# Kernel tuning notes

Measured on AMD Instinct MI355X. Metric: run time of the kernel, lower is better.

The kernel has to match this reference:

```python
import jax, jax.numpy as jnp
import numpy as np

L, H, D, DH, N, B, V, PAD = 6, 8, 512, 64, 300, 64, 32000, 0
DFF = 4 * D

def _layernorm(x, g, b):
    m = x.mean(-1, keepdims=True)
    v = ((x - m) ** 2).mean(-1, keepdims=True)
    return (x - m) * jax.lax.rsqrt(v + 1e-5) * g + b

def setup_inputs() -> dict:
    key = jax.random.key(0)
    ks = jax.random.split(key, 8)
    emb = jax.random.normal(ks[0], (V, D), dtype=jnp.float32) * 0.02
    emb = emb.at[PAD].set(0.0)  # padding_idx row is zero
    pos = jax.random.normal(ks[1], (N, D), dtype=jnp.float32) * 0.02
    Wk = jax.random.normal(ks[2], (L, H, D, DH), dtype=jnp.float32) * 0.02  # shared K=Q=V proj (module bug: uses self.key for all three)
    Wo = jax.random.normal(ks[3], (L, D, D), dtype=jnp.float32) * 0.02
    W1 = jax.random.normal(ks[4], (L, D, DFF), dtype=jnp.float32) * 0.02
    b1 = jnp.zeros((L, DFF), dtype=jnp.float32)
    W2 = jax.random.normal(ks[5], (L, DFF, D), dtype=jnp.float32) * 0.02
    b2 = jnp.zeros((L, D), dtype=jnp.float32)
    gamma = jnp.ones((L, D), dtype=jnp.float32)   # ONE LayerNorm per block, shared for both norms
    beta = jnp.zeros((L, D), dtype=jnp.float32)
    tokens = jax.random.randint(ks[6], (B, N), 0, V)
    return dict(tokens=tokens, emb=emb, pos=pos, Wk=Wk, Wo=Wo, W1=W1, b1=b1, W2=W2, b2=b2, gamma=gamma, beta=beta)

def reference(tokens, emb, pos, Wk, Wo, W1, b1, W2, b2, gamma, beta):
    x = emb[tokens] + pos[: tokens.shape[1]]  # [B,N,D]
    scale = 1.0 / jnp.sqrt(jnp.asarray(D, x.dtype))  # divides by sqrt(512), NOT sqrt(head_dim)
    for l in range(L):
        k = jnp.einsum('bnd,hde->bhne', x, Wk[l])          # Q=K=V  [B,H,N,DH]
        s = jnp.einsum('bhne,bhme->bhnm', k, k) * scale    # [B,H,N,N]
        a = jax.nn.softmax(s, axis=-1)
        o = jnp.einsum('bhnm,bhme->bhne', a, k)            # [B,H,N,DH]
        o = o.transpose(0, 2, 1, 3).reshape(x.shape[0], x.shape[1], D)
        z = _layernorm(o @ Wo[l] + x, gamma[l], beta[l])
        h = jax.nn.relu(z @ W1[l] + b1[l]) @ W2[l] + b2[l]
        x = _layernorm(h + z, gamma[l], beta[l])
    return x
```

## Files before the change

### kernel.cpp

```cpp
#include <hip/hip_runtime.h>

#define L_LAYERS 6
#define HEADS    8
#define DMODEL   512
#define DHEAD    64
#define SEQ      300
#define BATCH    64
#define DFFN     2048
#define BN_ROWS  (BATCH*SEQ)
#define NPAD     320

typedef __bf16 bf16_t;
typedef bf16_t bf16x8 __attribute__((ext_vector_type(8)));
typedef bf16_t bf16x4 __attribute__((ext_vector_type(4)));
typedef float  f32x4  __attribute__((ext_vector_type(4)));

#define GLOAD16(gp, lp) __builtin_amdgcn_global_load_lds( \
    (__attribute__((address_space(1))) void*)(gp),        \
    (__attribute__((address_space(3))) void*)(lp), 16, 0, 0)

__global__ __launch_bounds__(256) void transpose_w8(const float* __restrict__ w,
                                                    bf16_t* __restrict__ o,
                                                    int K, int Nc)
{
    int idx = blockIdx.x * 256 + threadIdx.x;
    int n   = idx % Nc;
    int r   = idx / Nc;
    int k8  = (r % (K / 8)) * 8;
    int l   = r / (K / 8);
    const float* wp = w + (size_t)l * K * Nc + (size_t)k8 * Nc + n;
    bf16x8 t;
#pragma unroll
    for (int j = 0; j < 8; ++j) t[j] = (bf16_t)wp[(size_t)j * Nc];
    *(bf16x8*)(o + (size_t)l * K * Nc + (size_t)n * K + k8) = t;
}

__global__ __launch_bounds__(256) void transpose_wk8(const float* __restrict__ wk,
                                                     bf16_t* __restrict__ o)
{
    int idx = blockIdx.x * 256 + threadIdx.x;
    int e  = idx % DHEAD;
    int r  = idx / DHEAD;
    int d8 = (r % (DMODEL / 8)) * 8;
    r      = r / (DMODEL / 8);
    int h  = r % HEADS;
    int l  = r / HEADS;
    const float* wp = wk + (((size_t)(l * HEADS + h) * DMODEL + d8) * DHEAD + e);
    bf16x8 t;
#pragma unroll
    for (int j = 0; j < 8; ++j) t[j] = (bf16_t)wp[(size_t)j * DHEAD];
    *(bf16x8*)(o + (size_t)l * DMODEL * DMODEL + (size_t)(h * DHEAD + e) * DMODEL + d8) = t;
}

__global__ __launch_bounds__(128) void embed_k(const int* __restrict__ tok,
                                               const float* __restrict__ emb,
                                               const float* __restrict__ pos,
                                               bf16_t* __restrict__ xb)
{
    int row = blockIdx.x;
    int n   = row % SEQ;
    int tkn = tok[row];
    int c   = threadIdx.x * 4;
    float4 e = *(const float4*)(emb + (size_t)tkn * DMODEL + c);
    float4 p = *(const float4*)(pos + (size_t)n * DMODEL + c);
    bf16x4 o;
    o[0] = (bf16_t)(e.x + p.x); o[1] = (bf16_t)(e.y + p.y);
    o[2] = (bf16_t)(e.z + p.z); o[3] = (bf16_t)(e.w + p.w);
    *(bf16x4*)(xb + (size_t)row * DMODEL + c) = o;
}

template <int EPI, typename OUT_T>
__global__ __launch_bounds__(256) void gemm_bt(const bf16_t* __restrict__ A,
                                               const bf16_t* __restrict__ BT,
                                               OUT_T* __restrict__ C,
                                               const float* __restrict__ bias,
                                               const bf16_t* __restrict__ resid,
                                               int M, int K, int Nc, int tiles_n)
{
    __shared__ bf16_t As[128 * 64];
    __shared__ bf16_t Bs[128 * 64];
    const int t    = threadIdx.x;
    const int tm   = blockIdx.x / tiles_n;
    const int tn   = blockIdx.x % tiles_n;
    const int lane = t & 63, wid = t >> 6;
    const int wr   = wid >> 1, wc = wid & 1;
    const int fr   = lane & 15, fq = lane >> 4;

    const f32x4 FZ = {0.f, 0.f, 0.f, 0.f};
    f32x4 acc[4][4];
#pragma unroll
    for (int m = 0; m < 4; ++m)
#pragma unroll
        for (int n = 0; n < 4; ++n) acc[m][n] = FZ;

    const bf16_t* Ab = A  + (size_t)tm * 128 * K;
    const bf16_t* Bb = BT + (size_t)tn * 128 * K;

    for (int k0 = 0; k0 < K; k0 += 64) {
#pragma unroll
        for (int i = 0; i < 4; ++i) {
            int idx8 = (i * 256 + t) * 8;
            int row  = idx8 >> 6;
            int colg = (idx8 & 63) ^ ((row & 7) << 3);
            GLOAD16(Ab + (size_t)row * K + k0 + colg, As + idx8);
            GLOAD16(Bb + (size_t)row * K + k0 + colg, Bs + idx8);
        }
        __syncthreads();
#pragma unroll
        for (int kk = 0; kk < 2; ++kk) {
            bf16x8 af[4], bfr[4];
#pragma unroll
            for (int m = 0; m < 4; ++m) {
                int row = wr * 64 + m * 16 + fr;
                af[m] = *(const bf16x8*)(As + row * 64 + ((kk * 32 + fq * 8) ^ ((row & 7) << 3)));
            }
#pragma unroll
            for (int n = 0; n < 4; ++n) {
                int row = wc * 64 + n * 16 + fr;
                bfr[n] = *(const bf16x8*)(Bs + row * 64 + ((kk * 32 + fq * 8) ^ ((row & 7) << 3)));
            }
#pragma unroll
            for (int m = 0; m < 4; ++m)
#pragma unroll
                for (int n = 0; n < 4; ++n)
                    acc[m][n] = __builtin_amdgcn_mfma_f32_16x16x32_bf16(af[m], bfr[n], acc[m][n], 0, 0, 0);
        }
        __syncthreads();
    }

#pragma unroll
    for (int m = 0; m < 4; ++m) {
#pragma unroll
        for (int n = 0; n < 4; ++n) {
            int colg = tn * 128 + wc * 64 + n * 16 + fr;
            float bv = (EPI == 2 || EPI == 3) ? bias[colg] : 0.f;
#pragma unroll
            for (int r = 0; r < 4; ++r) {
                int rowg = tm * 128 + wr * 64 + m * 16 + fq * 4 + r;
                float v = acc[m][n][r] + bv;
                if (EPI == 2) v = fmaxf(v, 0.f);
                if (EPI == 1 || EPI == 3) v += (float)resid[(size_t)rowg * Nc + colg];
                C[(size_t)rowg * Nc + colg] = (OUT_T)v;
            }
        }
    }
}

__global__ __launch_bounds__(256) void attn_k(const bf16_t* __restrict__ kin,
                                              bf16_t* __restrict__ out)
{
    __shared__ bf16_t Kl[NPAD * 64];
    __shared__ bf16_t KT[64 * NPAD];
    __shared__ bf16_t Pl[4 * 16 * NPAD];

    const int bh = blockIdx.x;
    const int b  = bh >> 3, h = bh & 7;
    const bf16_t* kbase = kin + (size_t)b * SEQ * DMODEL + h * DHEAD;
    const int t  = threadIdx.x;
    const int rr = t >> 3;
    const int cg = (t & 7) * 8;

    for (int pass = 0; pass < NPAD / 32; ++pass) {
        int row = pass * 32 + rr;
        bf16x8 v;
        if (row < SEQ) v = *(const bf16x8*)(kbase + (size_t)row * DMODEL + cg);
        else {
#pragma unroll
            for (int j = 0; j < 8; ++j) v[j] = (bf16_t)0.f;
        }
        *(bf16x8*)(Kl + row * 64 + (cg ^ ((row & 7) << 3))) = v;
#pragma unroll
        for (int j = 0; j < 8; ++j) {
            int col = cg + j;
            KT[col * NPAD + (row ^ ((col & 7) << 3))] = v[j];
        }
    }
    __syncthreads();

    const int lane = t & 63, w = t >> 6;
    const int fr = lane & 15, fq = lane >> 4;
    const float scale = 0.044194173824159216f;
    const f32x4 FZ = {0.f, 0.f, 0.f, 0.f};

    for (int i = 0; i < 5; ++i) {
        int qt = w * 5 + i;
        f32x4 s[20];
#pragma unroll
        for (int ct = 0; ct < 20; ++ct) s[ct] = FZ;
#pragma unroll
        for (int kk = 0; kk < 2; ++kk) {
            int qrow = qt * 16 + fr;
            bf16x8 aq = *(const bf16x8*)(Kl + qrow * 64 + ((kk * 32 + fq * 8) ^ ((qrow & 7) << 3)));
#pragma unroll
            for (int ct = 0; ct < 20; ++ct) {
                int krow = ct * 16 + fr;
                bf16x8 bk = *(const bf16x8*)(Kl + krow * 64 + ((kk * 32 + fq * 8) ^ ((krow & 7) << 3)));
                s[ct] = __builtin_amdgcn_mfma_f32_16x16x32_bf16(aq, bk, s[ct], 0, 0, 0);
            }
        }
#pragma unroll
        for (int r = 0; r < 4; ++r) {
            float mx = -1e30f;
#pragma unroll
            for (int ct = 0; ct < 20; ++ct) {
                float v = s[ct][r] * scale;
                if (ct * 16 + fr < SEQ) mx = fmaxf(mx, v);
            }
            mx = fmaxf(mx, __shfl_xor(mx, 1));
            mx = fmaxf(mx, __shfl_xor(mx, 2));
            mx = fmaxf(mx, __shfl_xor(mx, 4));
            mx = fmaxf(mx, __shfl_xor(mx, 8));
            float p[20];
            float sm = 0.f;
#pragma unroll
            for (int ct = 0; ct < 20; ++ct) {
                float v = (ct * 16 + fr < SEQ) ? __expf(s[ct][r] * scale - mx) : 0.f;
                p[ct] = v; sm += v;
            }
            sm += __shfl_xor(sm, 1); sm += __shfl_xor(sm, 2);
            sm += __shfl_xor(sm, 4); sm += __shfl_xor(sm, 8);
            float rinv = 1.f / sm;
            int pr = fq * 4 + r;
#pragma unroll
            for (int ct = 0; ct < 20; ++ct) {
                int col = ct * 16 + fr;
                Pl[(w * 16 + pr) * NPAD + (col ^ ((pr & 7) << 3))] = (bf16_t)(p[ct] * rinv);
            }
        }
#pragma unroll
        for (int n = 0; n < 4; ++n) {
            f32x4 oacc = FZ;
#pragma unroll
            for (int kk = 0; kk < 10; ++kk) {
                bf16x8 ap = *(const bf16x8*)(Pl + (w * 16 + fr) * NPAD + ((kk * 32 + fq * 8) ^ ((fr & 7) << 3)));
                int dr = n * 16 + fr;
                bf16x8 bv = *(const bf16x8*)(KT + dr * NPAD + ((kk * 32 + fq * 8) ^ ((dr & 7) << 3)));
                oacc = __builtin_amdgcn_mfma_f32_16x16x32_bf16(ap, bv, oacc, 0, 0, 0);
            }
#pragma unroll
            for (int r = 0; r < 4; ++r) {
                int qrow = qt * 16 + fq * 4 + r;
                if (qrow < SEQ)
                    out[(size_t)(b * SEQ + qrow) * DMODEL + h * DHEAD + n * 16 + fr] = (bf16_t)oacc[r];
            }
        }
    }
}

template <bool FINAL>
__global__ __launch_bounds__(256) void ln_k(const float* __restrict__ in,
                                            const float* __restrict__ gam,
                                            const float* __restrict__ bet,
                                            bf16_t* __restrict__ outb,
                                            float* __restrict__ outf)
{
    int row  = blockIdx.x * 4 + (threadIdx.x >> 6);
    int lane = threadIdx.x & 63;
    const float* x = in + (size_t)row * DMODEL + lane * 8;
    float4 v0 = *(const float4*)x;
    float4 v1 = *(const float4*)(x + 4);
    float s  = v0.x + v0.y + v0.z + v0.w + v1.x + v1.y + v1.z + v1.w;
    float s2 = v0.x * v0.x + v0.y * v0.y + v0.z * v0.z + v0.w * v0.w
             + v1.x * v1.x + v1.y * v1.y + v1.z * v1.z + v1.w * v1.w;
#pragma unroll
    for (int m = 1; m < 64; m <<= 1) { s += __shfl_xor(s, m); s2 += __shfl_xor(s2, m); }
    float mean = s * (1.f / DMODEL);
    float rstd = rsqrtf(s2 * (1.f / DMODEL) - mean * mean + 1e-5f);
    float4 g0 = *(const float4*)(gam + lane * 8), g1 = *(const float4*)(gam + lane * 8 + 4);
    float4 b0 = *(const float4*)(bet + lane * 8), b1 = *(const float4*)(bet + lane * 8 + 4);
    float y[8];
    y[0] = (v0.x - mean) * rstd * g0.x + b0.x;
    y[1] = (v0.y - mean) * rstd * g0.y + b0.y;
    y[2] = (v0.z - mean) * rstd * g0.z + b0.z;
    y[3] = (v0.w - mean) * rstd * g0.w + b0.w;
    y[4] = (v1.x - mean) * rstd * g1.x + b1.x;
    y[5] = (v1.y - mean) * rstd * g1.y + b1.y;
    y[6] = (v1.z - mean) * rstd * g1.z + b1.z;
    y[7] = (v1.w - mean) * rstd * g1.w + b1.w;
    bf16x8 ob;
#pragma unroll
    for (int j = 0; j < 8; ++j) ob[j] = (bf16_t)y[j];
    *(bf16x8*)(outb + (size_t)row * DMODEL + lane * 8) = ob;
    if (FINAL) {
        float4 o0 = {y[0], y[1], y[2], y[3]};
        float4 o1 = {y[4], y[5], y[6], y[7]};
        *(float4*)(outf + (size_t)row * DMODEL + lane * 8)     = o0;
        *(float4*)(outf + (size_t)row * DMODEL + lane * 8 + 4) = o1;
    }
}

extern "C" void kernel_launch(void* const* d_in, const int* in_sizes, int n_in,
                              void* d_out, int out_size, void* d_ws, size_t ws_size,
                              hipStream_t stream)
{
    const int*   tok = (const int*)d_in[0];
    const float* emb = (const float*)d_in[1];
    const float* pos = (const float*)d_in[2];
    const float* Wk  = (const float*)d_in[3];
    const float* Wo  = (const float*)d_in[4];
    const float* W1  = (const float*)d_in[5];
    const float* b1  = (const float*)d_in[6];
    const float* W2  = (const float*)d_in[7];
    const float* b2  = (const float*)d_in[8];
    const float* gam = (const float*)d_in[9];
    const float* bet = (const float*)d_in[10];
    float* outp = (float*)d_out;

    char* ws = (char*)d_ws;
    size_t off = 0;
    auto alloc = [&](size_t bytes) {
        off = (off + 255) & ~(size_t)255;
        void* p = ws + off;
        off += bytes;
        return p;
    };
    bf16_t* WKT  = (bf16_t*)alloc((size_t)L_LAYERS * DMODEL * DMODEL * 2);
    bf16_t* WOT  = (bf16_t*)alloc((size_t)L_LAYERS * DMODEL * DMODEL * 2);
    bf16_t* W1T  = (bf16_t*)alloc((size_t)L_LAYERS * DMODEL * DFFN * 2);
    bf16_t* W2T  = (bf16_t*)alloc((size_t)L_LAYERS * DMODEL * DFFN * 2);
    bf16_t* buf0 = (bf16_t*)alloc((size_t)BN_ROWS * DMODEL * 2);
    bf16_t* buf1 = (bf16_t*)alloc((size_t)BN_ROWS * DMODEL * 2);
    bf16_t* kb   = (bf16_t*)alloc((size_t)BN_ROWS * DMODEL * 2);
    bf16_t* ob   = (bf16_t*)alloc((size_t)BN_ROWS * DMODEL * 2);
    bf16_t* h1b  = (bf16_t*)alloc((size_t)BN_ROWS * DFFN * 2);
    float*  tf   = (float*)alloc((size_t)BN_ROWS * DMODEL * 4);

    transpose_wk8<<<768, 256, 0, stream>>>(Wk, WKT);
    transpose_w8<<<768, 256, 0, stream>>>(Wo, WOT, DMODEL, DMODEL);
    transpose_w8<<<3072, 256, 0, stream>>>(W1, W1T, DMODEL, DFFN);
    transpose_w8<<<3072, 256, 0, stream>>>(W2, W2T, DFFN, DMODEL);

    embed_k<<<BN_ROWS, 128, 0, stream>>>(tok, emb, pos, buf0);

    for (int l = 0; l < L_LAYERS; ++l) {
        gemm_bt<0, bf16_t><<<150 * 4, 256, 0, stream>>>(
            buf0, WKT + (size_t)l * DMODEL * DMODEL, kb, nullptr, nullptr,
            BN_ROWS, DMODEL, DMODEL, 4);
        attn_k<<<BATCH * HEADS, 256, 0, stream>>>(kb, ob);
        gemm_bt<1, float><<<150 * 4, 256, 0, stream>>>(
            ob, WOT + (size_t)l * DMODEL * DMODEL, tf, nullptr, buf0,
            BN_ROWS, DMODEL, DMODEL, 4);
        ln_k<false><<<BN_ROWS / 4, 256, 0, stream>>>(
            tf, gam + l * DMODEL, bet + l * DMODEL, buf1, nullptr);
        gemm_bt<2, bf16_t><<<150 * 16, 256, 0, stream>>>(
            buf1, W1T + (size_t)l * DMODEL * DFFN, h1b, b1 + l * DFFN, nullptr,
            BN_ROWS, DMODEL, DFFN, 16);
        gemm_bt<3, float><<<150 * 4, 256, 0, stream>>>(
            h1b, W2T + (size_t)l * DMODEL * DFFN, tf, b2 + l * DMODEL, buf1,
            BN_ROWS, DFFN, DMODEL, 4);
        if (l < L_LAYERS - 1)
            ln_k<false><<<BN_ROWS / 4, 256, 0, stream>>>(
                tf, gam + l * DMODEL, bet + l * DMODEL, buf0, nullptr);
        else
            ln_k<true><<<BN_ROWS / 4, 256, 0, stream>>>(
                tf, gam + l * DMODEL, bet + l * DMODEL, buf0, outp);
    }
}
```

Measured before the change: 1.786 ms.

## Replace GEMM with 256x256-tile double-buffered pipelined kernel and XCD-aware tile mapping

Replaces the 128x128 single-buffered GEMM with a 512-thread, 256x256-tile kernel that double-buffers A and B in LDS. Loads for the next K-tile are issued in phases interleaved with MFMA work, using explicit vmcnt waits, barriers and setprio. It also remaps block IDs so contiguous tiles land on the same XCD, and uses larger tiles to raise per-block data reuse. The cost is 128KB of LDS per block and fewer blocks: grids drop to 150 or 600 on a 256-CU part, which risks under-filling the GPU on the narrow GEMMs.

```diff
diff --git a/kernel.cpp b/kernel.cpp
--- a/kernel.cpp
+++ b/kernel.cpp
@@ -18,6 +18,10 @@
 #define GLOAD16(gp, lp) __builtin_amdgcn_global_load_lds( \
     (__attribute__((address_space(1))) void*)(gp),        \
     (__attribute__((address_space(3))) void*)(lp), 16, 0, 0)
+
+#define MEMBAR() asm volatile("" ::: "memory")
+#define PHASE_BAR() do { MEMBAR(); __builtin_amdgcn_s_barrier(); MEMBAR(); } while (0)
+#define VMCNT4() asm volatile("s_waitcnt vmcnt(4)" ::: "memory")
 
 __global__ __launch_bounds__(256) void transpose_w8(const float* __restrict__ w,
                                                     bf16_t* __restrict__ o,
@@ -70,77 +74,111 @@
 }
 
 template <int EPI, typename OUT_T>
-__global__ __launch_bounds__(256) void gemm_bt(const bf16_t* __restrict__ A,
-                                               const bf16_t* __restrict__ BT,
-                                               OUT_T* __restrict__ C,
-                                               const float* __restrict__ bias,
-                                               const bf16_t* __restrict__ resid,
-                                               int M, int K, int Nc, int tiles_n)
-{
-    __shared__ bf16_t As[128 * 64];
-    __shared__ bf16_t Bs[128 * 64];
-    const int t    = threadIdx.x;
-    const int tm   = blockIdx.x / tiles_n;
-    const int tn   = blockIdx.x % tiles_n;
+__global__ __launch_bounds__(512, 2) void gemm256(const bf16_t* __restrict__ A,
+                                                  const bf16_t* __restrict__ BT,
+                                                  OUT_T* __restrict__ C,
+                                                  const float* __restrict__ bias,
+                                                  const bf16_t* __restrict__ resid,
+                                                  int K, int Nc, int tiles_n)
+{
+    __shared__ bf16_t smem[65536];
+    bf16_t* As  = smem;
+    bf16_t* Bsm = smem + 32768;
+
+    const int t = threadIdx.x;
+    const int nwg = gridDim.x;
+    const int q = nwg >> 3, r = nwg & 7;
+    const int xc = blockIdx.x & 7, sq = blockIdx.x >> 3;
+    const int lt = (xc < r ? xc * (q + 1) : r * (q + 1) + (xc - r) * q) + sq;
+    const int tm = lt / tiles_n, tn = lt % tiles_n;
+
+    const bf16_t* Ab = A  + (size_t)tm * 256 * K;
+    const bf16_t* Bb = BT + (size_t)tn * 256 * K;
     const int lane = t & 63, wid = t >> 6;
-    const int wr   = wid >> 1, wc = wid & 1;
-    const int fr   = lane & 15, fq = lane >> 4;
+    const int wr = wid >> 2, wc = wid & 3;
+    const int fr = lane & 15, fq = lane >> 4;
+    const int NT = K >> 6;
+
+    auto stage_a = [&](int dbuf, int half, int kt) {
+#pragma unroll
+        for (int j = 0; j < 2; ++j) {
+            int idx8 = (j * 512 + t) * 8;
+            int rl   = idx8 >> 6;
+            int cg   = (idx8 & 63) ^ ((rl & 7) << 3);
+            GLOAD16(Ab + (size_t)(half * 128 + rl) * K + kt * 64 + cg,
+                    As + dbuf * 16384 + half * 8192 + idx8);
+        }
+    };
+    auto stage_b = [&](int dbuf, int nq, int kt) {
+#pragma unroll
+        for (int j = 0; j < 2; ++j) {
+            int idx8 = (j * 512 + t) * 8;
+            int rl   = idx8 >> 6;
+            int cg   = (idx8 & 63) ^ ((rl & 7) << 3);
+            int grow = (rl >> 5) * 64 + nq * 32 + (rl & 31);
+            GLOAD16(Bb + (size_t)grow * K + kt * 64 + cg,
+                    Bsm + dbuf * 16384 + nq * 8192 + idx8);
+        }
+    };
 
     const f32x4 FZ = {0.f, 0.f, 0.f, 0.f};
-    f32x4 acc[4][4];
-#pragma unroll
-    for (int m = 0; m < 4; ++m)
+    f32x4 acc[8][4];
+#pragma unroll
+    for (int m = 0; m < 8; ++m)
 #pragma unroll
         for (int n = 0; n < 4; ++n) acc[m][n] = FZ;
 
-    const bf16_t* Ab = A  + (size_t)tm * 128 * K;
-    const bf16_t* Bb = BT + (size_t)tn * 128 * K;
-
-    for (int k0 = 0; k0 < K; k0 += 64) {
-#pragma unroll
-        for (int i = 0; i < 4; ++i) {
-            int idx8 = (i * 256 + t) * 8;
-            int row  = idx8 >> 6;
-            int colg = (idx8 & 63) ^ ((row & 7) << 3);
-            GLOAD16(Ab + (size_t)row * K + k0 + colg, As + idx8);
-            GLOAD16(Bb + (size_t)row * K + k0 + colg, Bs + idx8);
-        }
-        __syncthreads();
-#pragma unroll
-        for (int kk = 0; kk < 2; ++kk) {
-            bf16x8 af[4], bfr[4];
-#pragma unroll
-            for (int m = 0; m < 4; ++m) {
-                int row = wr * 64 + m * 16 + fr;
-                af[m] = *(const bf16x8*)(As + row * 64 + ((kk * 32 + fq * 8) ^ ((row & 7) << 3)));
-            }
-#pragma unroll
-            for (int n = 0; n < 4; ++n) {
-                int row = wc * 64 + n * 16 + fr;
-                bfr[n] = *(const bf16x8*)(Bs + row * 64 + ((kk * 32 + fq * 8) ^ ((row & 7) << 3)));
-            }
-#pragma unroll
-            for (int m = 0; m < 4; ++m)
-#pragma unroll
-                for (int n = 0; n < 4; ++n)
-                    acc[m][n] = __builtin_amdgcn_mfma_f32_16x16x32_bf16(af[m], bfr[n], acc[m][n], 0, 0, 0);
-        }
-        __syncthreads();
-    }
-
-#pragma unroll
-    for (int m = 0; m < 4; ++m) {
+    stage_a(0, 0, 0); stage_a(0, 1, 0);
+    stage_b(0, 0, 0); stage_b(0, 1, 0);
+    stage_b(1, 0, 1);
+    VMCNT4();
+    PHASE_BAR();
+
+    for (int tt = 0; tt < NT; ++tt) {
+        const int buf = tt & 1, nbuf = buf ^ 1;
+        const bf16_t* Ap = As + buf * 16384 + (wr * 128 + fr) * 64;
+#pragma unroll
+        for (int ph = 0; ph < 4; ++ph) {
+            const int nq = ph >> 1, kk = ph & 1;
+            const int ca = (kk * 32 + fq * 8) ^ ((fr & 7) << 3);
+            bf16x8 af[8];
+#pragma unroll
+            for (int m = 0; m < 8; ++m)
+                af[m] = *(const bf16x8*)(Ap + m * 1024 + ca);
+            const bf16_t* Bp = Bsm + buf * 16384 + nq * 8192 + (wc * 32 + fr) * 64;
+            bf16x8 b0 = *(const bf16x8*)(Bp + ca);
+            bf16x8 b1 = *(const bf16x8*)(Bp + 1024 + ca);
+
+            if (ph == 0) { if (tt + 1 < NT) stage_a(nbuf, 0, tt + 1); }
+            if (ph == 1) { if (tt + 1 < NT) stage_a(nbuf, 1, tt + 1); VMCNT4(); }
+            if (ph == 2) { if (tt + 2 < NT) stage_b(buf, 0, tt + 2); }
+            if (ph == 3) { if (tt + 1 < NT) stage_b(nbuf, 1, tt + 1); VMCNT4(); }
+
+            PHASE_BAR();
+            __builtin_amdgcn_s_setprio(1);
+#pragma unroll
+            for (int m = 0; m < 8; ++m) {
+                acc[m][nq * 2]     = __builtin_amdgcn_mfma_f32_16x16x32_bf16(af[m], b0, acc[m][nq * 2], 0, 0, 0);
+                acc[m][nq * 2 + 1] = __builtin_amdgcn_mfma_f32_16x16x32_bf16(af[m], b1, acc[m][nq * 2 + 1], 0, 0, 0);
+            }
+            __builtin_amdgcn_s_setprio(0);
+            PHASE_BAR();
+        }
+    }
+
+#pragma unroll
+    for (int m = 0; m < 8; ++m) {
+        const int rowg = tm * 256 + wr * 128 + m * 16 + fq * 4;
 #pragma unroll
         for (int n = 0; n < 4; ++n) {
-            int colg = tn * 128 + wc * 64 + n * 16 + fr;
+            const int colg = tn * 256 + wc * 64 + n * 16 + fr;
             float bv = (EPI == 2 || EPI == 3) ? bias[colg] : 0.f;
 #pragma unroll
-            for (int r = 0; r < 4; ++r) {
-                int rowg = tm * 128 + wr * 64 + m * 16 + fq * 4 + r;
-                float v = acc[m][n][r] + bv;
+            for (int rr = 0; rr < 4; ++rr) {
+                float v = acc[m][n][rr] + bv;
                 if (EPI == 2) v = fmaxf(v, 0.f);
-                if (EPI == 1 || EPI == 3) v += (float)resid[(size_t)rowg * Nc + colg];
-                C[(size_t)rowg * Nc + colg] = (OUT_T)v;
+                if (EPI == 1 || EPI == 3) v += (float)resid[(size_t)(rowg + rr) * Nc + colg];
+                C[(size_t)(rowg + rr) * Nc + colg] = (OUT_T)v;
             }
         }
     }
@@ -333,21 +371,21 @@
     embed_k<<<BN_ROWS, 128, 0, stream>>>(tok, emb, pos, buf0);
 
     for (int l = 0; l < L_LAYERS; ++l) {
-        gemm_bt<0, bf16_t><<<150 * 4, 256, 0, stream>>>(
+        gemm256<0, bf16_t><<<75 * 2, 512, 0, stream>>>(
             buf0, WKT + (size_t)l * DMODEL * DMODEL, kb, nullptr, nullptr,
-            BN_ROWS, DMODEL, DMODEL, 4);
+            DMODEL, DMODEL, 2);
         attn_k<<<BATCH * HEADS, 256, 0, stream>>>(kb, ob);
-        gemm_bt<1, float><<<150 * 4, 256, 0, stream>>>(
+        gemm256<1, float><<<75 * 2, 512, 0, stream>>>(
             ob, WOT + (size_t)l * DMODEL * DMODEL, tf, nullptr, buf0,
-            BN_ROWS, DMODEL, DMODEL, 4);
+            DMODEL, DMODEL, 2);
         ln_k<false><<<BN_ROWS / 4, 256, 0, stream>>>(
             tf, gam + l * DMODEL, bet + l * DMODEL, buf1, nullptr);
-        gemm_bt<2, bf16_t><<<150 * 16, 256, 0, stream>>>(
+        gemm256<2, bf16_t><<<75 * 8, 512, 0, stream>>>(
             buf1, W1T + (size_t)l * DMODEL * DFFN, h1b, b1 + l * DFFN, nullptr,
-            BN_ROWS, DMODEL, DFFN, 16);
-        gemm_bt<3, float><<<150 * 4, 256, 0, stream>>>(
+            DMODEL, DFFN, 8);
+        gemm256<3, float><<<75 * 2, 512, 0, stream>>>(
             h1b, W2T + (size_t)l * DMODEL * DFFN, tf, b2 + l * DMODEL, buf1,
-            BN_ROWS, DFFN, DMODEL, 4);
+            DFFN, DMODEL, 2);
         if (l < L_LAYERS - 1)
             ln_k<false><<<BN_ROWS / 4, 256, 0, stream>>>(
                 tf, gam + l * DMODEL, bet + l * DMODEL, buf0, nullptr);
```

New measurement: 1.692 ms. 1.06x faster.

## Double-buffer GEMM LDS loads, remap tiles across XCDs, store pre-LN sums as bf16

Applied to the files above, without the earlier changes.

The GEMM now double-buffers its LDS tiles, so the next K-slice's global-to-LDS loads are issued while the current slice's MFMAs run, and one barrier per iteration replaces two. It also raises MFMA wave priority, sets two blocks per SM through launch bounds, and remaps block IDs so contiguous tiles land on the same XCD for L2 reuse. Separately, the residual-add output feeding LayerNorm is stored as bf16 instead of fp32, which halves that intermediate traffic. That adds extra rounding before the normalization.

```diff
diff --git a/kernel.cpp b/kernel.cpp
--- a/kernel.cpp
+++ b/kernel.cpp
@@ -18,6 +18,10 @@
 #define GLOAD16(gp, lp) __builtin_amdgcn_global_load_lds( \
     (__attribute__((address_space(1))) void*)(gp),        \
     (__attribute__((address_space(3))) void*)(lp), 16, 0, 0)
+
+#define MEMBAR() asm volatile("" ::: "memory")
+#define PHASE_BAR() do { MEMBAR(); __builtin_amdgcn_s_barrier(); MEMBAR(); } while (0)
+#define VMCNT0() asm volatile("s_waitcnt vmcnt(0)" ::: "memory")
 
 __global__ __launch_bounds__(256) void transpose_w8(const float* __restrict__ w,
                                                     bf16_t* __restrict__ o,
@@ -70,21 +74,40 @@
 }
 
 template <int EPI, typename OUT_T>
-__global__ __launch_bounds__(256) void gemm_bt(const bf16_t* __restrict__ A,
-                                               const bf16_t* __restrict__ BT,
-                                               OUT_T* __restrict__ C,
-                                               const float* __restrict__ bias,
-                                               const bf16_t* __restrict__ resid,
-                                               int M, int K, int Nc, int tiles_n)
-{
-    __shared__ bf16_t As[128 * 64];
-    __shared__ bf16_t Bs[128 * 64];
-    const int t    = threadIdx.x;
-    const int tm   = blockIdx.x / tiles_n;
-    const int tn   = blockIdx.x % tiles_n;
+__global__ __launch_bounds__(256, 2) void gemm128(const bf16_t* __restrict__ A,
+                                                  const bf16_t* __restrict__ BT,
+                                                  OUT_T* __restrict__ C,
+                                                  const float* __restrict__ bias,
+                                                  const bf16_t* __restrict__ resid,
+                                                  int K, int Nc, int tiles_n)
+{
+    __shared__ bf16_t smem[32768];
+    bf16_t* As = smem;
+    bf16_t* Bs = smem + 16384;
+
+    const int t = threadIdx.x;
+    const int nwg = gridDim.x;
+    const int q = nwg >> 3, r = nwg & 7;
+    const int xc = blockIdx.x & 7, sq = blockIdx.x >> 3;
+    const int lt = (xc < r ? xc * (q + 1) : r * (q + 1) + (xc - r) * q) + sq;
+    const int tm = lt / tiles_n, tn = lt % tiles_n;
+
+    const bf16_t* Ab = A  + (size_t)tm * 128 * K;
+    const bf16_t* Bb = BT + (size_t)tn * 128 * K;
     const int lane = t & 63, wid = t >> 6;
-    const int wr   = wid >> 1, wc = wid & 1;
-    const int fr   = lane & 15, fq = lane >> 4;
+    const int wr = wid >> 1, wc = wid & 1;
+    const int fr = lane & 15, fq = lane >> 4;
+    const int NT = K >> 6;
+
+    auto stage = [&](bf16_t* dst, const bf16_t* src, int kt) {
+#pragma unroll
+        for (int j = 0; j < 4; ++j) {
+            int idx8 = (j * 256 + t) * 8;
+            int rl   = idx8 >> 6;
+            int cg   = (idx8 & 63) ^ ((rl & 7) << 3);
+            GLOAD16(src + (size_t)rl * K + kt * 64 + cg, dst + idx8);
+        }
+    };
 
     const f32x4 FZ = {0.f, 0.f, 0.f, 0.f};
     f32x4 acc[4][4];
@@ -93,39 +116,40 @@
 #pragma unroll
         for (int n = 0; n < 4; ++n) acc[m][n] = FZ;
 
-    const bf16_t* Ab = A  + (size_t)tm * 128 * K;
-    const bf16_t* Bb = BT + (size_t)tn * 128 * K;
-
-    for (int k0 = 0; k0 < K; k0 += 64) {
-#pragma unroll
-        for (int i = 0; i < 4; ++i) {
-            int idx8 = (i * 256 + t) * 8;
-            int row  = idx8 >> 6;
-            int colg = (idx8 & 63) ^ ((row & 7) << 3);
-            GLOAD16(Ab + (size_t)row * K + k0 + colg, As + idx8);
-            GLOAD16(Bb + (size_t)row * K + k0 + colg, Bs + idx8);
-        }
-        __syncthreads();
-#pragma unroll
-        for (int kk = 0; kk < 2; ++kk) {
-            bf16x8 af[4], bfr[4];
-#pragma unroll
-            for (int m = 0; m < 4; ++m) {
-                int row = wr * 64 + m * 16 + fr;
-                af[m] = *(const bf16x8*)(As + row * 64 + ((kk * 32 + fq * 8) ^ ((row & 7) << 3)));
-            }
-#pragma unroll
-            for (int n = 0; n < 4; ++n) {
-                int row = wc * 64 + n * 16 + fr;
-                bfr[n] = *(const bf16x8*)(Bs + row * 64 + ((kk * 32 + fq * 8) ^ ((row & 7) << 3)));
-            }
-#pragma unroll
-            for (int m = 0; m < 4; ++m)
-#pragma unroll
-                for (int n = 0; n < 4; ++n)
-                    acc[m][n] = __builtin_amdgcn_mfma_f32_16x16x32_bf16(af[m], bfr[n], acc[m][n], 0, 0, 0);
-        }
-        __syncthreads();
+    stage(As, Ab, 0); stage(Bs, Bb, 0);
+    VMCNT0(); PHASE_BAR();
+
+    for (int tt = 0; tt < NT; ++tt) {
+        const int buf = tt & 1, nbuf = buf ^ 1;
+        const bf16_t* Ap = As + buf * 8192 + (wr * 64 + fr) * 64;
+        const bf16_t* Bp = Bs + buf * 8192 + (wc * 64 + fr) * 64;
+        const int ca0 = (fq * 8) ^ ((fr & 7) << 3);
+        const int ca1 = ca0 ^ 32;
+        bf16x8 af[4], bfr[4];
+#pragma unroll
+        for (int m = 0; m < 4; ++m) af[m] = *(const bf16x8*)(Ap + m * 1024 + ca0);
+#pragma unroll
+        for (int n = 0; n < 4; ++n) bfr[n] = *(const bf16x8*)(Bp + n * 1024 + ca0);
+        if (tt + 1 < NT) { stage(As + nbuf * 8192, Ab, tt + 1); stage(Bs + nbuf * 8192, Bb, tt + 1); }
+        __builtin_amdgcn_s_setprio(1);
+#pragma unroll
+        for (int m = 0; m < 4; ++m)
+#pragma unroll
+            for (int n = 0; n < 4; ++n)
+                acc[m][n] = __builtin_amdgcn_mfma_f32_16x16x32_bf16(af[m], bfr[n], acc[m][n], 0, 0, 0);
+        __builtin_amdgcn_s_setprio(0);
+#pragma unroll
+        for (int m = 0; m < 4; ++m) af[m] = *(const bf16x8*)(Ap + m * 1024 + ca1);
+#pragma unroll
+        for (int n = 0; n < 4; ++n) bfr[n] = *(const bf16x8*)(Bp + n * 1024 + ca1);
+        __builtin_amdgcn_s_setprio(1);
+#pragma unroll
+        for (int m = 0; m < 4; ++m)
+#pragma unroll
+            for (int n = 0; n < 4; ++n)
+                acc[m][n] = __builtin_amdgcn_mfma_f32_16x16x32_bf16(af[m], bfr[n], acc[m][n], 0, 0, 0);
+        __builtin_amdgcn_s_setprio(0);
+        VMCNT0(); PHASE_BAR();
     }
 
 #pragma unroll
@@ -135,9 +159,9 @@
             int colg = tn * 128 + wc * 64 + n * 16 + fr;
             float bv = (EPI == 2 || EPI == 3) ? bias[colg] : 0.f;
 #pragma unroll
-            for (int r = 0; r < 4; ++r) {
-                int rowg = tm * 128 + wr * 64 + m * 16 + fq * 4 + r;
-                float v = acc[m][n][r] + bv;
+            for (int rr2 = 0; rr2 < 4; ++rr2) {
+                int rowg = tm * 128 + wr * 64 + m * 16 + fq * 4 + rr2;
+                float v = acc[m][n][rr2] + bv;
                 if (EPI == 2) v = fmaxf(v, 0.f);
                 if (EPI == 1 || EPI == 3) v += (float)resid[(size_t)rowg * Nc + colg];
                 C[(size_t)rowg * Nc + colg] = (OUT_T)v;
@@ -248,7 +272,7 @@
 }
 
 template <bool FINAL>
-__global__ __launch_bounds__(256) void ln_k(const float* __restrict__ in,
+__global__ __launch_bounds__(256) void ln_k(const bf16_t* __restrict__ in,
                                             const float* __restrict__ gam,
                                             const float* __restrict__ bet,
                                             bf16_t* __restrict__ outb,
@@ -256,34 +280,36 @@
 {
     int row  = blockIdx.x * 4 + (threadIdx.x >> 6);
     int lane = threadIdx.x & 63;
-    const float* x = in + (size_t)row * DMODEL + lane * 8;
-    float4 v0 = *(const float4*)x;
-    float4 v1 = *(const float4*)(x + 4);
-    float s  = v0.x + v0.y + v0.z + v0.w + v1.x + v1.y + v1.z + v1.w;
-    float s2 = v0.x * v0.x + v0.y * v0.y + v0.z * v0.z + v0.w * v0.w
-             + v1.x * v1.x + v1.y * v1.y + v1.z * v1.z + v1.w * v1.w;
+    bf16x8 v = *(const bf16x8*)(in + (size_t)row * DMODEL + lane * 8);
+    float y[8];
+    float s = 0.f, s2 = 0.f;
+#pragma unroll
+    for (int j = 0; j < 8; ++j) {
+        float f = (float)v[j];
+        y[j] = f; s += f; s2 += f * f;
+    }
 #pragma unroll
     for (int m = 1; m < 64; m <<= 1) { s += __shfl_xor(s, m); s2 += __shfl_xor(s2, m); }
     float mean = s * (1.f / DMODEL);
     float rstd = rsqrtf(s2 * (1.f / DMODEL) - mean * mean + 1e-5f);
     float4 g0 = *(const float4*)(gam + lane * 8), g1 = *(const float4*)(gam + lane * 8 + 4);
     float4 b0 = *(const float4*)(bet + lane * 8), b1 = *(const float4*)(bet + lane * 8 + 4);
-    float y[8];
-    y[0] = (v0.x - mean) * rstd * g0.x + b0.x;
-    y[1] = (v0.y - mean) * rstd * g0.y + b0.y;
-    y[2] = (v0.z - mean) * rstd * g0.z + b0.z;
-    y[3] = (v0.w - mean) * rstd * g0.w + b0.w;
-    y[4] = (v1.x - mean) * rstd * g1.x + b1.x;
-    y[5] = (v1.y - mean) * rstd * g1.y + b1.y;
-    y[6] = (v1.z - mean) * rstd * g1.z + b1.z;
-    y[7] = (v1.w - mean) * rstd * g1.w + b1.w;
+    float z[8];
+    z[0] = (y[0] - mean) * rstd * g0.x + b0.x;
+    z[1] = (y[1] - mean) * rstd * g0.y + b0.y;
+    z[2] = (y[2] - mean) * rstd * g0.z + b0.z;
+    z[3] = (y[3] - mean) * rstd * g0.w + b0.w;
+    z[4] = (y[4] - mean) * rstd * g1.x + b1.x;
+    z[5] = (y[5] - mean) * rstd * g1.y + b1.y;
+    z[6] = (y[6] - mean) * rstd * g1.z + b1.z;
+    z[7] = (y[7] - mean) * rstd * g1.w + b1.w;
     bf16x8 ob;
 #pragma unroll
-    for (int j = 0; j < 8; ++j) ob[j] = (bf16_t)y[j];
+    for (int j = 0; j < 8; ++j) ob[j] = (bf16_t)z[j];
     *(bf16x8*)(outb + (size_t)row * DMODEL + lane * 8) = ob;
     if (FINAL) {
-        float4 o0 = {y[0], y[1], y[2], y[3]};
-        float4 o1 = {y[4], y[5], y[6], y[7]};
+        float4 o0 = {z[0], z[1], z[2], z[3]};
+        float4 o1 = {z[4], z[5], z[6], z[7]};
         *(float4*)(outf + (size_t)row * DMODEL + lane * 8)     = o0;
         *(float4*)(outf + (size_t)row * DMODEL + lane * 8 + 4) = o1;
     }
@@ -323,7 +349,7 @@
     bf16_t* kb   = (bf16_t*)alloc((size_t)BN_ROWS * DMODEL * 2);
     bf16_t* ob   = (bf16_t*)alloc((size_t)BN_ROWS * DMODEL * 2);
     bf16_t* h1b  = (bf16_t*)alloc((size_t)BN_ROWS * DFFN * 2);
-    float*  tf   = (float*)alloc((size_t)BN_ROWS * DMODEL * 4);
+    bf16_t* tfb  = (bf16_t*)alloc((size_t)BN_ROWS * DMODEL * 2);
 
     transpose_wk8<<<768, 256, 0, stream>>>(Wk, WKT);
     transpose_w8<<<768, 256, 0, stream>>>(Wo, WOT, DMODEL, DMODEL);
@@ -333,26 +359,26 @@
     embed_k<<<BN_ROWS, 128, 0, stream>>>(tok, emb, pos, buf0);
 
     for (int l = 0; l < L_LAYERS; ++l) {
-        gemm_bt<0, bf16_t><<<150 * 4, 256, 0, stream>>>(
+        gemm128<0, bf16_t><<<600, 256, 0, stream>>>(
             buf0, WKT + (size_t)l * DMODEL * DMODEL, kb, nullptr, nullptr,
-            BN_ROWS, DMODEL, DMODEL, 4);
+            DMODEL, DMODEL, 4);
         attn_k<<<BATCH * HEADS, 256, 0, stream>>>(kb, ob);
-        gemm_bt<1, float><<<150 * 4, 256, 0, stream>>>(
-            ob, WOT + (size_t)l * DMODEL * DMODEL, tf, nullptr, buf0,
-            BN_ROWS, DMODEL, DMODEL, 4);
+        gemm128<1, bf16_t><<<600, 256, 0, stream>>>(
+            ob, WOT + (size_t)l * DMODEL * DMODEL, tfb, nullptr, buf0,
+            DMODEL, DMODEL, 4);
         ln_k<false><<<BN_ROWS / 4, 256, 0, stream>>>(
-            tf, gam + l * DMODEL, bet + l * DMODEL, buf1, nullptr);
-        gemm_bt<2, bf16_t><<<150 * 16, 256, 0, stream>>>(
+            tfb, gam + l * DMODEL, bet + l * DMODEL, buf1, nullptr);
+        gemm128<2, bf16_t><<<2400, 256, 0, stream>>>(
             buf1, W1T + (size_t)l * DMODEL * DFFN, h1b, b1 + l * DFFN, nullptr,
-            BN_ROWS, DMODEL, DFFN, 16);
-        gemm_bt<3, float><<<150 * 4, 256, 0, stream>>>(
-            h1b, W2T + (size_t)l * DMODEL * DFFN, tf, b2 + l * DMODEL, buf1,
-            BN_ROWS, DFFN, DMODEL, 4);
+            DMODEL, DFFN, 16);
+        gemm128<3, bf16_t><<<600, 256, 0, stream>>>(
+            h1b, W2T + (size_t)l * DMODEL * DFFN, tfb, b2 + l * DMODEL, buf1,
+            DFFN, DMODEL, 4);
         if (l < L_LAYERS - 1)
             ln_k<false><<<BN_ROWS / 4, 256, 0, stream>>>(
-                tf, gam + l * DMODEL, bet + l * DMODEL, buf0, nullptr);
+                tfb, gam + l * DMODEL, bet + l * DMODEL, buf0, nullptr);
         else
             ln_k<true><<<BN_ROWS / 4, 256, 0, stream>>>(
-                tf, gam + l * DMODEL, bet + l * DMODEL, buf0, outp);
-    }
-}
+                tfb, gam + l * DMODEL, bet + l * DMODEL, buf0, outp);
+    }
+}
```

Result: faster. 1.530 ms (-14.3%).
